# Kernel optimization log

Measured on AMD Instinct MI355X. Metric: run time of the kernel, lower is better.

The kernel has to match this reference:

```python
import jax, jax.numpy as jnp
import numpy as np

BLOCK = 256


def setup_inputs() -> dict:
    key = jax.random.key(0)
    ks = jax.random.split(key, 6)
    b, n, hid = 2, 4096, 2048
    h, d = 16, 128
    x = jax.random.normal(ks[0], (b, n, hid), dtype=jnp.float32)
    slope_rate = jax.random.uniform(ks[1], (h, 1, 1), dtype=jnp.float32)
    Wqkv = jax.random.normal(ks[2], (3 * h * d, hid), dtype=jnp.float32) * 0.02
    Wg = jax.random.normal(ks[3], (h * d, hid), dtype=jnp.float32) * 0.02
    norm_w = jnp.ones((h * d,), dtype=jnp.float32)
    Wo = jax.random.normal(ks[4], (hid, h * d), dtype=jnp.float32) * 0.02
    return {"x": x, "slope_rate": slope_rate, "Wqkv": Wqkv, "Wg": Wg, "norm_w": norm_w, "Wo": Wo}


def reference(x, slope_rate, Wqkv, Wg, norm_w, Wo):
    b, n, hid = x.shape
    h = slope_rate.shape[0]
    d = Wqkv.shape[0] // (3 * h)
    nb = n // BLOCK

    qkv = jax.nn.silu(x @ Wqkv.T).reshape(b, n, h, 3 * d)
    q, k, v = jnp.split(qkv, 3, axis=-1)           # each (b, n, h, d)
    # -> (b, h, n, d)
    q = q.transpose(0, 2, 1, 3)
    k = k.transpose(0, 2, 1, 3)
    v = v.transpose(0, 2, 1, 3)

    s = slope_rate.astype(jnp.float32)             # (h, 1, 1)
    arr = jnp.arange(1, BLOCK + 1, dtype=jnp.float32)
    q_decay = jnp.exp(-s * arr[:, None])           # (h, BLOCK, 1)
    k_decay = jnp.exp(-s * (BLOCK - arr[:, None])) # (h, BLOCK, 1)
    idx = arr[:, None] - arr[None, :]              # (BLOCK, BLOCK)
    diag_decay = jnp.where(idx >= 0, jnp.exp(-s * idx), 0.0)  # (h, BLOCK, BLOCK)
    block_decay = jnp.exp(-s * BLOCK)              # (h, 1, 1)

    # chunk into blocks: (nb, b, h, BLOCK, d)
    def chunk(t):
        return t.reshape(b, h, nb, BLOCK, d).transpose(2, 0, 1, 3, 4)
    qc, kc, vc = chunk(q), chunk(k), chunk(v)

    def step(kv, qkv_blk):
        qi, ki, vi = qkv_blk
        # inter-block: decayed query against running kv state
        out_nd = jnp.einsum('bhmd,bhde->bhme', qi * q_decay, kv)
        # intra-block: decay-masked quadratic attention
        qk = jnp.einsum('bhmd,bhnd->bhmn', qi, ki) * diag_decay
        out_d = jnp.einsum('bhmn,bhne->bhme', qk, vi)
        kv_new = block_decay * kv + jnp.einsum('bhmd,bhme->bhde', ki * k_decay, vi)
        return kv_new, out_nd + out_d

    kv0 = jnp.zeros((b, h, d, d), dtype=jnp.float32)
    _, out_blocks = jax.lax.scan(step, kv0, (qc, kc, vc))  # (nb, b, h, BLOCK, d)

    out = out_blocks.transpose(1, 2, 0, 3, 4).reshape(b, h, n, d)
    out = out.transpose(0, 2, 1, 3).reshape(b, n, h * d)  # b n (h d)

    # RMSNorm
    eps = jnp.finfo(jnp.float32).eps
    rms = jax.lax.rsqrt(jnp.mean(out * out, axis=-1, keepdims=True) + eps)
    out = out * rms * norm_w

    gate = jax.nn.sigmoid(x @ Wg.T)
    return (gate * out) @ Wo.T
```

## Files before the change

kernel.cpp:

```cpp
#include <hip/hip_runtime.h>
#include <stdint.h>

typedef __attribute__((ext_vector_type(8))) short short8;
typedef __attribute__((ext_vector_type(4))) float f32x4;

#define DEV static __device__ __forceinline__

DEV float b2f(unsigned short u) {
  unsigned x = ((unsigned)u) << 16;
  return __builtin_bit_cast(float, x);
}
DEV unsigned short f2b(float f) {
  unsigned x = __builtin_bit_cast(unsigned, f);
  return (unsigned short)((x + 0x7fffu + ((x >> 16) & 1u)) >> 16);
}
DEV void gload16(const unsigned short* g, unsigned short* l) {
  __builtin_amdgcn_global_load_lds((const __attribute__((address_space(1))) void*)g,
                                   (__attribute__((address_space(3))) void*)l, 16, 0, 0);
}
#define MFMA(a, b, c) __builtin_amdgcn_mfma_f32_16x16x32_bf16(a, b, c, 0, 0, 0)
#define BARRIER                          \
  asm volatile("" ::: "memory");         \
  __builtin_amdgcn_s_barrier();          \
  asm volatile("" ::: "memory")

__global__ void k_f2b(const float* __restrict__ in, unsigned short* __restrict__ out, long n) {
  long i = ((long)blockIdx.x * blockDim.x + threadIdx.x) * 4;
  long stride = (long)gridDim.x * blockDim.x * 4;
  for (; i < n; i += stride) {
    float4 f = *(const float4*)(in + i);
    ushort4 o;
    o.x = f2b(f.x); o.y = f2b(f.y); o.z = f2b(f.z); o.w = f2b(f.w);
    *(ushort4*)(out + i) = o;
  }
}

template <int MODE>
__global__ __launch_bounds__(512, 2) void k_gemm(
    const unsigned short* __restrict__ A, const unsigned short* __restrict__ B0,
    const unsigned short* __restrict__ B1,
    unsigned short* __restrict__ o_q, unsigned short* __restrict__ o_k,
    unsigned short* __restrict__ o_v, unsigned short* __restrict__ o_g,
    float* __restrict__ o_f) {
  const int K = 2048, NT = 32;
  __shared__ unsigned short sm[65536];
  int tid = threadIdx.x, w = tid >> 6, lane = tid & 63;
  int wm = w >> 2, wn = w & 3;
  int l15 = lane & 15, l4 = lane >> 4;
  int xcd = blockIdx.x & 7, sub = blockIdx.x >> 3;
  int tm = xcd * 4 + (sub & 3), tn = sub >> 2;
  int brow = tm << 8, bcol = tn << 8;
  const unsigned short* Ab = A + (size_t)brow * K;
  const unsigned short* Bb = (MODE == 1 || bcol < 6144) ? (B0 + (size_t)bcol * K)
                                                        : (B1 + (size_t)(bcol - 6144) * K);
  f32x4 acc[8][4];
#pragma unroll
  for (int m = 0; m < 8; m++)
#pragma unroll
    for (int n = 0; n < 4; n++) acc[m][n] = (f32x4)0.f;

  auto stageU = [&](int TT, int s) {
    int tsrc = TT < NT ? TT : NT - 1;
    unsigned short* lb = sm + (TT & 1) * 32768 + s * 8192;
    int kt = tsrc << 6;
    const unsigned short* gb = (s & 1) ? Bb : Ab;
    int ro = (s >> 1) << 7;
#pragma unroll
    for (int i = 0; i < 2; ++i) {
      int c = i * 512 + tid;
      int pos = c >> 3, pb = c & 7;
      gload16(gb + (size_t)(ro + pos) * K + kt + ((pb ^ (pos & 7)) << 3), lb + c * 8);
    }
  };

  stageU(0, 0); stageU(0, 1); stageU(0, 3); stageU(0, 2);
  stageU(1, 0); stageU(1, 1); stageU(1, 3);
  asm volatile("s_waitcnt vmcnt(8)" ::: "memory");
  BARRIER;

  const int bslot = (wn >> 1) ? 3 : 1;
  const int bposb = (wn & 1) * 64;

  for (int T = 0; T < NT; ++T) {
    const unsigned short* bufb = sm + (T & 1) * 32768;
    const unsigned short* Bslot = bufb + bslot * 8192;
    short8 af[4][2], bfr[2][2][2];

    auto ldA = [&](const unsigned short* base) {
#pragma unroll
      for (int mi = 0; mi < 4; ++mi) {
        int pos = wm * 64 + mi * 16 + l15;
#pragma unroll
        for (int ks = 0; ks < 2; ++ks)
          af[mi][ks] = *(const short8*)(base + pos * 64 + (((ks * 4 + l4) ^ (pos & 7)) << 3));
      }
    };
    auto ldB = [&](int nh) {
#pragma unroll
      for (int nj = 0; nj < 2; ++nj) {
        int pos = bposb + nh * 32 + nj * 16 + l15;
#pragma unroll
        for (int ks = 0; ks < 2; ++ks)
          bfr[nh][nj][ks] = *(const short8*)(Bslot + pos * 64 + (((ks * 4 + l4) ^ (pos & 7)) << 3));
      }
    };
    auto mfmaQ = [&](int mh, int nh) {
      __builtin_amdgcn_s_setprio(1);
#pragma unroll
      for (int mi = 0; mi < 4; ++mi)
#pragma unroll
        for (int nj = 0; nj < 2; ++nj)
#pragma unroll
          for (int ks = 0; ks < 2; ++ks)
            acc[mh * 4 + mi][nh * 2 + nj] =
                MFMA(af[mi][ks], bfr[nh][nj][ks], acc[mh * 4 + mi][nh * 2 + nj]);
      __builtin_amdgcn_s_setprio(0);
    };

    ldA(bufb);
    ldB(0);
    stageU(T + 1, 2);
    BARRIER;
    mfmaQ(0, 0);
    BARRIER;
    ldB(1);
    stageU(T + 2, 0);
    BARRIER;
    mfmaQ(0, 1);
    asm volatile("s_waitcnt vmcnt(10)" ::: "memory");
    BARRIER;
    ldA(bufb + 2 * 8192);
    stageU(T + 2, 1);
    stageU(T + 2, 3);
    BARRIER;
    mfmaQ(1, 1);
    BARRIER;
    mfmaQ(1, 0);
    asm volatile("s_waitcnt vmcnt(8)" ::: "memory");
    BARRIER;
  }

#pragma unroll
  for (int mf = 0; mf < 8; ++mf)
#pragma unroll
    for (int r = 0; r < 4; ++r) {
      int row = brow + (mf >> 2) * 128 + wm * 64 + (mf & 3) * 16 + l4 * 4 + r;
#pragma unroll
      for (int ni = 0; ni < 4; ++ni) {
        int col = bcol + wn * 64 + ni * 16 + l15;
        float v = acc[mf][ni][r];
        if (MODE == 0) {
          if (col < 6144) {
            float sv = v / (1.f + __expf(-v));
            int h = col / 384, dd = col - h * 384;
            int b = row >> 12, t = row & 4095;
            size_t base = ((size_t)(b * 16 + h) * 4096 + t) * 128;
            if (dd < 128) o_q[base + dd] = f2b(sv);
            else if (dd < 256) o_k[base + dd - 128] = f2b(sv);
            else o_v[base + dd - 256] = f2b(sv);
          } else {
            float gv = 1.f / (1.f + __expf(-v));
            o_g[(size_t)row * 2048 + (col - 6144)] = f2b(gv);
          }
        } else {
          o_f[(size_t)row * 2048 + col] = v;
        }
      }
    }
}

__global__ __launch_bounds__(256) void k_kvblk(const unsigned short* __restrict__ kk,
                                               const unsigned short* __restrict__ vv,
                                               const float* __restrict__ slope,
                                               unsigned short* __restrict__ kvT) {
  int gid = blockIdx.x;
  int bh = gid >> 4, blk = gid & 15;
  float s = slope[bh & 15];
  __shared__ unsigned short kT[128][72];
  __shared__ unsigned short vT[128][72];
  int tid = threadIdx.x, w = tid >> 6, lane = tid & 63;
  int wrow = (w >> 1) * 64, wcol = (w & 1) * 64;
  f32x4 acc[4][4];
#pragma unroll
  for (int m = 0; m < 4; m++)
#pragma unroll
    for (int n = 0; n < 4; n++) acc[m][n] = (f32x4)0.f;
  const unsigned short* kb = kk + ((size_t)bh * 4096 + blk * 256) * 128;
  const unsigned short* vb = vv + ((size_t)bh * 4096 + blk * 256) * 128;
  int tt = tid & 63, c0 = (tid >> 6) * 32;
  for (int tc = 0; tc < 4; ++tc) {
    __syncthreads();
    int tg = tc * 64 + tt;
    float kd = __expf(-s * (float)(255 - tg));
#pragma unroll
    for (int g = 0; g < 4; ++g) {
      int c = c0 + g * 8;
      short8 k8 = *(const short8*)(kb + (size_t)tg * 128 + c);
      short8 v8 = *(const short8*)(vb + (size_t)tg * 128 + c);
#pragma unroll
      for (int j = 0; j < 8; ++j) {
        kT[c + j][tt] = f2b(b2f((unsigned short)k8[j]) * kd);
        vT[c + j][tt] = (unsigned short)v8[j];
      }
    }
    __syncthreads();
#pragma unroll
    for (int kx = 0; kx < 64; kx += 32) {
      int ko = kx + (lane >> 4) * 8;
      short8 af[4], bfr[4];
#pragma unroll
      for (int m = 0; m < 4; m++) af[m] = *(const short8*)&vT[wrow + m * 16 + (lane & 15)][ko];
#pragma unroll
      for (int n = 0; n < 4; n++) bfr[n] = *(const short8*)&kT[wcol + n * 16 + (lane & 15)][ko];
#pragma unroll
      for (int m = 0; m < 4; m++)
#pragma unroll
        for (int n = 0; n < 4; n++) acc[m][n] = MFMA(af[m], bfr[n], acc[m][n]);
    }
  }
  unsigned short* op = kvT + (size_t)gid * 16384;
#pragma unroll
  for (int m = 0; m < 4; m++)
#pragma unroll
    for (int r = 0; r < 4; r++) {
      int e = wrow + m * 16 + (lane >> 4) * 4 + r;
#pragma unroll
      for (int n = 0; n < 4; n++) {
        int d = wcol + n * 16 + (lane & 15);
        op[e * 128 + d] = f2b(acc[m][n][r]);
      }
    }
}

__global__ void k_scan(unsigned short* kvT, const float* __restrict__ slope) {
  int gid = blockIdx.x;
  int bh = gid >> 6;
  int eo = (gid & 63) * 256 + threadIdx.x;
  float s = slope[bh & 15];
  float bd = __expf(-s * 256.f);
  float st = 0.f;
  size_t base = (size_t)bh * 16 * 16384 + eo;
#pragma unroll
  for (int i = 0; i < 16; ++i) {
    unsigned short c = kvT[base + (size_t)i * 16384];
    kvT[base + (size_t)i * 16384] = f2b(st);
    st = bd * st + b2f(c);
  }
}

__global__ __launch_bounds__(256) void k_attn(const unsigned short* __restrict__ q,
                                              const unsigned short* __restrict__ kk,
                                              const unsigned short* __restrict__ vv,
                                              const unsigned short* __restrict__ kvT,
                                              const float* __restrict__ slope,
                                              unsigned short* __restrict__ attn) {
  int gid = blockIdx.x;
  int hf = gid & 1, blk = (gid >> 1) & 15, bh = gid >> 5;
  float s = slope[bh & 15];
  __shared__ unsigned short k_sh[64][136];
  __shared__ unsigned short vT_sh[128][72];
  __shared__ unsigned short s_sh[4][32][72];
  int tid = threadIdx.x, w = tid >> 6, lane = tid & 63;
  int mm0 = hf * 128 + w * 32;
  const unsigned short* qb = q + ((size_t)bh * 4096 + blk * 256) * 128;
  const unsigned short* kvb = kvT + (size_t)(bh * 16 + blk) * 16384;
  f32x4 acc[2][8];
#pragma unroll
  for (int m = 0; m < 2; m++)
#pragma unroll
    for (int n = 0; n < 8; n++) acc[m][n] = (f32x4)0.f;
#pragma unroll
  for (int kx = 0; kx < 128; kx += 32) {
    int ko = kx + (lane >> 4) * 8;
    short8 af[2], bfr[8];
#pragma unroll
    for (int mi = 0; mi < 2; mi++)
      af[mi] = *(const short8*)(qb + (size_t)(mm0 + mi * 16 + (lane & 15)) * 128 + ko);
#pragma unroll
    for (int ni = 0; ni < 8; ni++)
      bfr[ni] = *(const short8*)(kvb + (size_t)(ni * 16 + (lane & 15)) * 128 + ko);
#pragma unroll
    for (int mi = 0; mi < 2; mi++)
#pragma unroll
      for (int ni = 0; ni < 8; ni++) acc[mi][ni] = MFMA(af[mi], bfr[ni], acc[mi][ni]);
  }
#pragma unroll
  for (int mi = 0; mi < 2; mi++)
#pragma unroll
    for (int r = 0; r < 4; r++) {
      float qd = __expf(-s * (float)(mm0 + mi * 16 + (lane >> 4) * 4 + r + 1));
#pragma unroll
      for (int ni = 0; ni < 8; ni++) acc[mi][ni][r] *= qd;
    }
  int nchunk = 2 * (hf + 1);
  for (int tc = 0; tc < nchunk; ++tc) {
    __syncthreads();
    {
      int t2 = tid >> 2, c = (tid & 3) * 32;
      const unsigned short* kp = kk + ((size_t)bh * 4096 + blk * 256 + tc * 64 + t2) * 128 + c;
#pragma unroll
      for (int g = 0; g < 4; ++g) *(short8*)&k_sh[t2][c + g * 8] = *(const short8*)(kp + g * 8);
    }
    {
      int t2 = tid & 63, e0 = (tid >> 6) * 32;
      const unsigned short* vp = vv + ((size_t)bh * 4096 + blk * 256 + tc * 64 + t2) * 128 + e0;
#pragma unroll
      for (int g = 0; g < 4; ++g) {
        short8 v8 = *(const short8*)(vp + g * 8);
#pragma unroll
        for (int j = 0; j < 8; ++j) vT_sh[e0 + g * 8 + j][t2] = (unsigned short)v8[j];
      }
    }
    __syncthreads();
    if (tc * 64 <= mm0 + 31) {
      f32x4 sa[2][4];
#pragma unroll
      for (int m = 0; m < 2; m++)
#pragma unroll
        for (int n = 0; n < 4; n++) sa[m][n] = (f32x4)0.f;
#pragma unroll
      for (int kx = 0; kx < 128; kx += 32) {
        int ko = kx + (lane >> 4) * 8;
        short8 af[2], bfr[4];
#pragma unroll
        for (int mi = 0; mi < 2; mi++)
          af[mi] = *(const short8*)(qb + (size_t)(mm0 + mi * 16 + (lane & 15)) * 128 + ko);
#pragma unroll
        for (int ni = 0; ni < 4; ni++) bfr[ni] = *(const short8*)&k_sh[ni * 16 + (lane & 15)][ko];
#pragma unroll
        for (int mi = 0; mi < 2; mi++)
#pragma unroll
          for (int ni = 0; ni < 4; ni++) sa[mi][ni] = MFMA(af[mi], bfr[ni], sa[mi][ni]);
      }
#pragma unroll
      for (int mi = 0; mi < 2; mi++)
#pragma unroll
        for (int ni = 0; ni < 4; ni++)
#pragma unroll
          for (int r = 0; r < 4; r++) {
            int mm = mm0 + mi * 16 + (lane >> 4) * 4 + r;
            int ttg = tc * 64 + ni * 16 + (lane & 15);
            int diff = mm - ttg;
            float val = (diff >= 0) ? sa[mi][ni][r] * __expf(-s * (float)diff) : 0.f;
            s_sh[w][mi * 16 + (lane >> 4) * 4 + r][ni * 16 + (lane & 15)] = f2b(val);
          }
#pragma unroll
      for (int k2 = 0; k2 < 64; k2 += 32) {
        int ko2 = k2 + (lane >> 4) * 8;
        short8 a2[2];
#pragma unroll
        for (int mi = 0; mi < 2; mi++)
          a2[mi] = *(const short8*)&s_sh[w][mi * 16 + (lane & 15)][ko2];
#pragma unroll
        for (int ni = 0; ni < 8; ni++) {
          short8 b2 = *(const short8*)&vT_sh[ni * 16 + (lane & 15)][ko2];
#pragma unroll
          for (int mi = 0; mi < 2; mi++) acc[mi][ni] = MFMA(a2[mi], b2, acc[mi][ni]);
        }
      }
    }
  }
  int b = bh >> 4, h = bh & 15;
#pragma unroll
  for (int mi = 0; mi < 2; mi++)
#pragma unroll
    for (int r = 0; r < 4; r++) {
      int mm = mm0 + mi * 16 + (lane >> 4) * 4 + r;
      size_t rowp = ((size_t)b * 4096 + blk * 256 + mm) * 2048 + h * 128;
#pragma unroll
      for (int ni = 0; ni < 8; ni++) attn[rowp + ni * 16 + (lane & 15)] = f2b(acc[mi][ni][r]);
    }
}

__global__ __launch_bounds__(256) void k_norm(const unsigned short* __restrict__ attn,
                                              const unsigned short* __restrict__ gate,
                                              const float* __restrict__ nw,
                                              unsigned short* __restrict__ y) {
  int row = blockIdx.x;
  int tid = threadIdx.x, w = tid >> 6, lane = tid & 63;
  const unsigned short* ap = attn + (size_t)row * 2048 + tid * 8;
  const unsigned short* gp = gate + (size_t)row * 2048 + tid * 8;
  short8 a8 = *(const short8*)ap;
  float vals[8];
  float ss = 0.f;
#pragma unroll
  for (int j = 0; j < 8; ++j) {
    vals[j] = b2f((unsigned short)a8[j]);
    ss += vals[j] * vals[j];
  }
#pragma unroll
  for (int off = 32; off > 0; off >>= 1) ss += __shfl_down(ss, off, 64);
  __shared__ float red[4];
  if (lane == 0) red[w] = ss;
  __syncthreads();
  float tot = red[0] + red[1] + red[2] + red[3];
  float rms = rsqrtf(tot * (1.f / 2048.f) + 1.1920929e-07f);
  short8 g8 = *(const short8*)gp;
  short8 o;
#pragma unroll
  for (int j = 0; j < 8; ++j)
    o[j] = (short)f2b(vals[j] * rms * nw[tid * 8 + j] * b2f((unsigned short)g8[j]));
  *(short8*)(y + (size_t)row * 2048 + tid * 8) = o;
}

extern "C" void kernel_launch(void* const* d_in, const int* in_sizes, int n_in, void* d_out,
                              int out_size, void* d_ws, size_t ws_size, hipStream_t stream) {
  const float* x = (const float*)d_in[0];
  const float* slope = (const float*)d_in[1];
  const float* Wqkv = (const float*)d_in[2];
  const float* Wg = (const float*)d_in[3];
  const float* nw = (const float*)d_in[4];
  const float* Wo = (const float*)d_in[5];
  float* out = (float*)d_out;

  unsigned short* q = (unsigned short*)d_ws;
  unsigned short* k = q + 16777216;
  unsigned short* v = k + 16777216;
  unsigned short* gate = v + 16777216;
  unsigned short* xb = gate + 16777216;
  unsigned short* wqkvb = xb + 16777216;
  unsigned short* wgb = wqkvb + 12582912;
  unsigned short* wob = wgb + 4194304;
  unsigned short* kvT = wob + 4194304;
  unsigned short* attn = wqkvb;
  unsigned short* y = xb;

  k_f2b<<<2048, 256, 0, stream>>>(x, xb, 16777216L);
  k_f2b<<<2048, 256, 0, stream>>>(Wqkv, wqkvb, 12582912L);
  k_f2b<<<1024, 256, 0, stream>>>(Wg, wgb, 4194304L);
  k_f2b<<<1024, 256, 0, stream>>>(Wo, wob, 4194304L);

  k_gemm<0><<<1024, 512, 0, stream>>>(xb, wqkvb, wgb, q, k, v, gate, nullptr);
  k_kvblk<<<512, 256, 0, stream>>>(k, v, slope, kvT);
  k_scan<<<2048, 256, 0, stream>>>(kvT, slope);
  k_attn<<<1024, 256, 0, stream>>>(q, k, v, kvT, slope, attn);
  k_norm<<<8192, 256, 0, stream>>>(attn, gate, nw, y);
  k_gemm<1><<<256, 512, 0, stream>>>(y, wob, nullptr, nullptr, nullptr, nullptr, nullptr, out);
}
```

Measured before the change: 520.8 us.

## Restructure GEMM main loop into two-phase schedule with prefetched A fragments

```diff
diff --git a/kernel.cpp b/kernel.cpp
--- a/kernel.cpp
+++ b/kernel.cpp
@@ -34,6 +34,16 @@
     *(ushort4*)(out + i) = o;
   }
 }
+
+#define LDFRAG(dst, base, posbase)                                                        \
+  {                                                                                       \
+    _Pragma("unroll") for (int fi = 0; fi < 4; ++fi) {                                    \
+      int pos = (posbase) + fi * 16 + l15;                                                \
+      _Pragma("unroll") for (int ks = 0; ks < 2; ++ks)                                    \
+          dst[fi][ks] =                                                                   \
+              *(const short8*)((base) + pos * 64 + (((ks * 4 + l4) ^ (pos & 7)) << 3));   \
+    }                                                                                     \
+  }
 
 template <int MODE>
 __global__ __launch_bounds__(512, 2) void k_gemm(
@@ -73,70 +83,46 @@
     }
   };
 
-  stageU(0, 0); stageU(0, 1); stageU(0, 3); stageU(0, 2);
-  stageU(1, 0); stageU(1, 1); stageU(1, 3);
-  asm volatile("s_waitcnt vmcnt(8)" ::: "memory");
-  BARRIER;
-
   const int bslot = (wn >> 1) ? 3 : 1;
   const int bposb = (wn & 1) * 64;
+  short8 afA[4][2], afB[4][2], bfr[4][2];
+
+  stageU(0, 0); stageU(0, 1); stageU(0, 3); stageU(0, 2);
+  asm volatile("s_waitcnt vmcnt(2)" ::: "memory");
+  BARRIER;
+  LDFRAG(afA, sm, wm * 64);
+  stageU(1, 0); stageU(1, 1); stageU(1, 3);
+  asm volatile("s_waitcnt vmcnt(6)" ::: "memory");
+  BARRIER;
 
   for (int T = 0; T < NT; ++T) {
-    const unsigned short* bufb = sm + (T & 1) * 32768;
-    const unsigned short* Bslot = bufb + bslot * 8192;
-    short8 af[4][2], bfr[2][2][2];
-
-    auto ldA = [&](const unsigned short* base) {
-#pragma unroll
-      for (int mi = 0; mi < 4; ++mi) {
-        int pos = wm * 64 + mi * 16 + l15;
+    const unsigned short* buf0 = sm + (T & 1) * 32768;
+    const unsigned short* buf1 = sm + ((T + 1) & 1) * 32768;
+    LDFRAG(bfr, buf0 + bslot * 8192, bposb);
+    LDFRAG(afB, buf0 + 2 * 8192, wm * 64);
+    stageU(T + 1, 2);
+    __builtin_amdgcn_s_setprio(1);
+#pragma unroll
+    for (int mi = 0; mi < 4; ++mi)
+#pragma unroll
+      for (int nj = 0; nj < 4; ++nj)
+#pragma unroll
+        for (int ks = 0; ks < 2; ++ks) acc[mi][nj] = MFMA(afA[mi][ks], bfr[nj][ks], acc[mi][nj]);
+    __builtin_amdgcn_s_setprio(0);
+    asm volatile("s_waitcnt vmcnt(2)" ::: "memory");
+    BARRIER;
+    LDFRAG(afA, buf1, wm * 64);
+    stageU(T + 2, 0); stageU(T + 2, 1); stageU(T + 2, 3);
+    __builtin_amdgcn_s_setprio(1);
+#pragma unroll
+    for (int mi = 0; mi < 4; ++mi)
+#pragma unroll
+      for (int nj = 0; nj < 4; ++nj)
 #pragma unroll
         for (int ks = 0; ks < 2; ++ks)
-          af[mi][ks] = *(const short8*)(base + pos * 64 + (((ks * 4 + l4) ^ (pos & 7)) << 3));
-      }
-    };
-    auto ldB = [&](int nh) {
-#pragma unroll
-      for (int nj = 0; nj < 2; ++nj) {
-        int pos = bposb + nh * 32 + nj * 16 + l15;
-#pragma unroll
-        for (int ks = 0; ks < 2; ++ks)
-          bfr[nh][nj][ks] = *(const short8*)(Bslot + pos * 64 + (((ks * 4 + l4) ^ (pos & 7)) << 3));
-      }
-    };
-    auto mfmaQ = [&](int mh, int nh) {
-      __builtin_amdgcn_s_setprio(1);
-#pragma unroll
-      for (int mi = 0; mi < 4; ++mi)
-#pragma unroll
-        for (int nj = 0; nj < 2; ++nj)
-#pragma unroll
-          for (int ks = 0; ks < 2; ++ks)
-            acc[mh * 4 + mi][nh * 2 + nj] =
-                MFMA(af[mi][ks], bfr[nh][nj][ks], acc[mh * 4 + mi][nh * 2 + nj]);
-      __builtin_amdgcn_s_setprio(0);
-    };
-
-    ldA(bufb);
-    ldB(0);
-    stageU(T + 1, 2);
-    BARRIER;
-    mfmaQ(0, 0);
-    BARRIER;
-    ldB(1);
-    stageU(T + 2, 0);
-    BARRIER;
-    mfmaQ(0, 1);
-    asm volatile("s_waitcnt vmcnt(10)" ::: "memory");
-    BARRIER;
-    ldA(bufb + 2 * 8192);
-    stageU(T + 2, 1);
-    stageU(T + 2, 3);
-    BARRIER;
-    mfmaQ(1, 1);
-    BARRIER;
-    mfmaQ(1, 0);
-    asm volatile("s_waitcnt vmcnt(8)" ::: "memory");
+          acc[4 + mi][nj] = MFMA(afB[mi][ks], bfr[nj][ks], acc[4 + mi][nj]);
+    __builtin_amdgcn_s_setprio(0);
+    asm volatile("s_waitcnt vmcnt(6)" ::: "memory");
     BARRIER;
   }
 
```

Result: no change. 512.9 us (-1.5%).
